# Kernel tuning notes

Hardware: AMD Instinct MI355X
Metric: run time of the kernel (lower is better)

## Reference

```python
import jax, jax.numpy as jnp
import numpy as np

N = 8192      # batch (subjects)
XD = 32       # covariate dim
LD = 32       # encoder latent dim
HD = 128      # odefunc hidden dim
TD = 3        # trans_dim (illness-death model)
NH = 3        # number_of_hazards (allowed transitions)
NP = TD * TD  # num_probs
G = 256       # time grid intervals -> 257 unique times incl. 0
DT = 0.01
STATE = 2 * NP + NH  # [P | P^-1 | cum hazards] = 21


def setup_inputs() -> dict:
    rng = np.random.default_rng(0)
    x = rng.standard_normal((N, XD)).astype(np.float32)
    times = (np.arange(G + 1) * DT).astype(np.float32)  # unique grid incl. t=0
    si = rng.integers(0, G, size=N)
    ei = si + 1 + (rng.random(N) * (G - si)).astype(np.int64)  # ei in (si, G]
    tstart = times[si]
    tstop = times[ei]
    fs = rng.integers(1, 3, size=N)  # from_state in {1,2}
    ts = np.where(fs == 1, rng.integers(2, 4, size=N), 3)  # valid transitions
    # allowed transitions of [[0,1,1],[0,0,1],[0,0,0]]
    trans_rows = np.array([0, 0, 1], dtype=np.int32)
    trans_cols = np.array([1, 2, 2], dtype=np.int32)

    def lin(k, fi, fo, s=1.0):
        r = np.random.default_rng(k)
        return (r.standard_normal((fi, fo)).astype(np.float32) * s / np.sqrt(fi),
                np.zeros(fo, dtype=np.float32))
    enc_W1, enc_b1 = lin(1, XD, 64)
    enc_W2, enc_b2 = lin(2, 64, LD)
    net_W1, net_b1 = lin(3, STATE + LD + XD + 1, HD)
    net_W2, net_b2 = lin(4, HD, 2 * NH, s=0.5)
    return {
        "x": jnp.asarray(x), "tstart": jnp.asarray(tstart), "tstop": jnp.asarray(tstop),
        "from_state": jnp.asarray(fs, jnp.int64), "to_state": jnp.asarray(ts, jnp.int64),
        "tstart_idx": jnp.asarray(si, jnp.int64), "tstop_idx": jnp.asarray(ei, jnp.int64),
        "times": jnp.asarray(times), "trans_rows": jnp.asarray(trans_rows),
        "trans_cols": jnp.asarray(trans_cols),
        "enc_W1": jnp.asarray(enc_W1), "enc_b1": jnp.asarray(enc_b1),
        "enc_W2": jnp.asarray(enc_W2), "enc_b2": jnp.asarray(enc_b2),
        "net_W1": jnp.asarray(net_W1), "net_b1": jnp.asarray(net_b1),
        "net_W2": jnp.asarray(net_W2), "net_b2": jnp.asarray(net_b2),
    }


def reference(x, tstart, tstop, from_state, to_state, tstart_idx, tstop_idx, times,
              trans_rows, trans_cols, enc_W1, enc_b1, enc_W2, enc_b2,
              net_W1, net_b1, net_W2, net_b2):
    n = x.shape[0]
    z = jnp.tanh(x @ enc_W1 + enc_b1) @ enc_W2 + enc_b2  # encoder(x): [n, LD]

    def net(h):  # odefunc.net
        return jnp.tanh(h @ net_W1 + net_b1) @ net_W2 + net_b2

    di = jnp.arange(TD)

    def qmat(qvec, with_diag):
        # scatter hazards into [n,3,3] transition-rate matrix (mask positions)
        Q = jnp.zeros((n, TD, TD), qvec.dtype).at[:, trans_rows, trans_cols].set(qvec)
        if with_diag:
            Q = Q.at[:, di, di].set(-jnp.sum(Q, axis=-1))
        return Q

    # ODE state: [ vec(P(0,t)) | vec(P(0,t)^-1) | cumulative hazards ]
    P0 = jnp.tile(jnp.eye(TD, dtype=x.dtype).reshape(-1), (n, 1))
    state0 = jnp.concatenate([P0, P0, jnp.zeros((n, NH), x.dtype)], axis=1)

    def deriv(state, t):
        P = state[:, :NP].reshape(n, TD, TD)
        Tinv = state[:, NP:2 * NP].reshape(n, TD, TD)
        h = jnp.concatenate([state, z, x, jnp.full((n, 1), t, x.dtype)], axis=1)
        qvec = jax.nn.softplus(net(h)[:, :NH])  # softplus_beta = 1
        Q = qmat(qvec, True)
        dP = jnp.einsum('nij,njk->nik', P, Q)      # dP/dt = P Q
        dTinv = -jnp.einsum('nij,njk->nik', Q, Tinv)  # d(P^-1)/dt = -Q P^-1
        return jnp.concatenate([dP.reshape(n, -1), dTinv.reshape(n, -1), qvec], axis=1)

    def step(state, tdt):
        t, dt = tdt
        new = state + dt * deriv(state, t)  # explicit Euler on the event grid
        return new, new

    dts = times[1:] - times[:-1]
    _, outs = jax.lax.scan(step, state0, (times[:-1], dts))
    out = jnp.concatenate([state0[None], outs], axis=0)  # [T, n, STATE]

    ar = jnp.arange(n)
    # vectorized replacement of the per-sample python-loop gathers
    Tinv_start = out[tstart_idx, ar, NP:2 * NP].reshape(n, TD, TD)
    T_stop = out[tstop_idx, ar, :NP].reshape(n, TD, TD)
    Sfull = jnp.einsum('nij,njk->nik', Tinv_start, T_stop)
    fi = from_state - 1
    ti = to_state - 1
    S = Sfull[ar, fi, fi]

    state_stop = out[tstop_idx, ar, :]
    h1 = jnp.concatenate([state_stop, z, x, tstop[:, None]], axis=1)
    qvec = jax.nn.softplus(net(h1)[:, :NH])
    q = qmat(qvec, False)  # forward() does NOT fill the diagonal here
    lam = q[ar, fi, ti]

    h2 = jnp.concatenate([out[-1], z, x, jnp.full((n, 1), jnp.max(tstop), x.dtype)], axis=1)
    all_hazards_T = net(h2)[:, NH:]
    return S, lam, all_hazards_T
```

## Files before the change

kernel.cpp:

```cpp
#include <hip/hip_runtime.h>

#define NSAMP 8192
#define GSTEP 256
#define SCL   2.8853900817779268f
#define L2E   1.4426950408889634f
#define LN2   0.69314718055994531f
#define LN2DT 0.0069314718055994531f

typedef __attribute__((ext_vector_type(8))) short short8;
typedef __attribute__((ext_vector_type(4))) float f32x4;

__device__ __forceinline__ float exp2_hw(float x){ float r; asm("v_exp_f32 %0, %1" : "=v"(r) : "v"(x)); return r; }
__device__ __forceinline__ float log2_hw(float x){ float r; asm("v_log_f32 %0, %1" : "=v"(r) : "v"(x)); return r; }
__device__ __forceinline__ unsigned pk_bf16(float a, float b){ unsigned r; asm("v_cvt_pk_bf16_f32 %0, %1, %2" : "=v"(r) : "v"(a), "v"(b)); return r; }

__device__ __forceinline__ float tanh_scl(float y) {
    float e = exp2_hw(y);
    return fmaf(-2.0f, __builtin_amdgcn_rcpf(1.0f + e), 1.0f);
}
__device__ __forceinline__ float fast_tanh(float x) {
    float e = exp2_hw(x * SCL);
    return fmaf(-2.0f, __builtin_amdgcn_rcpf(1.0f + e), 1.0f);
}

union frag_u { unsigned u[4]; short8 s; };

__device__ __forceinline__ void split8(const float* v, short8& H, short8& L) {
    frag_u Hu, Lu;
    #pragma unroll
    for (int r = 0; r < 4; ++r) {
        float a = v[2*r], b = v[2*r+1];
        unsigned h = pk_bf16(a, b);
        float ha = __int_as_float(h << 16);
        float hb = __int_as_float(h & 0xffff0000u);
        Hu.u[r] = h;
        Lu.u[r] = pk_bf16(a - ha, b - hb);
    }
    H = Hu.s; L = Lu.s;
}

__global__ void tmax_k(const float* __restrict__ tstop, float* __restrict__ ws) {
    __shared__ float sm[16];
    float m = -1e30f;
    for (int i = threadIdx.x; i < NSAMP; i += 1024) m = fmaxf(m, tstop[i]);
    #pragma unroll
    for (int o = 32; o > 0; o >>= 1) m = fmaxf(m, __shfl_down(m, o, 64));
    if ((threadIdx.x & 63) == 0) sm[threadIdx.x >> 6] = m;
    __syncthreads();
    if (threadIdx.x == 0) {
        float r = sm[0];
        for (int w = 1; w < 16; ++w) r = fmaxf(r, sm[w]);
        ws[0] = r;
    }
}

__global__ void enc_k(const float* __restrict__ x,
                      const float* __restrict__ eW1, const float* __restrict__ eb1,
                      const float* __restrict__ eW2, const float* __restrict__ eb2,
                      float* __restrict__ zout) {
    int s = blockIdx.x * 256 + threadIdx.x;
    float xv[32];
    #pragma unroll
    for (int i = 0; i < 8; ++i) {
        float4 v = reinterpret_cast<const float4*>(x)[s * 8 + i];
        xv[4*i+0] = v.x; xv[4*i+1] = v.y; xv[4*i+2] = v.z; xv[4*i+3] = v.w;
    }
    float z[32];
    #pragma unroll
    for (int o = 0; o < 32; ++o) z[o] = eb2[o];
    #pragma unroll 4
    for (int h = 0; h < 64; ++h) {
        float a = eb1[h];
        #pragma unroll
        for (int i = 0; i < 32; ++i) a += xv[i] * eW1[i * 64 + h];
        float th = fast_tanh(a);
        #pragma unroll
        for (int o = 0; o < 32; ++o) z[o] += th * eW2[h * 32 + o];
    }
    #pragma unroll
    for (int o = 0; o < 32; ++o) zout[s * 32 + o] = z[o];
}

__global__ void __launch_bounds__(64, 1)
surv_k(const float* __restrict__ x,
       const float* __restrict__ tstop,
       const int* __restrict__ fsv, const int* __restrict__ tsv,
       const int* __restrict__ siv, const int* __restrict__ eiv,
       const float* __restrict__ W1, const float* __restrict__ b1,
       const float* __restrict__ W2, const float* __restrict__ b2,
       const float* __restrict__ wsf,
       float* __restrict__ out)
{
    const int l   = threadIdx.x;
    const int a   = l >> 4;
    const int col = l & 15;
    const int s   = blockIdx.x * 16 + col;

    short8 A1h[8], A1l[8];
    #pragma unroll
    for (int tt = 0; tt < 8; ++tt) {
        float av[8];
        #pragma unroll
        for (int i = 0; i < 8; ++i) {
            int k = a * 8 + i;
            float v = 0.f;
            if (k < 21) v = W1[k * 128 + tt * 16 + col];
            else if (k == 21) v = W1[85 * 128 + tt * 16 + col];
            av[i] = v * SCL;
        }
        split8(av, A1h[tt], A1l[tt]);
    }

    short8 A2f[4];
    {
        int  cc  = (col < 6) ? col : 0;
        bool cok = (col < 6);
        float csc = (col < 3) ? L2E : 1.0f;
        #pragma unroll
        for (int j = 0; j < 4; ++j) {
            frag_u F;
            #pragma unroll
            for (int rr = 0; rr < 4; ++rr) {
                int e0 = 2 * rr, e1 = e0 + 1;
                int h0 = j * 32 + (e0 >> 2) * 16 + a * 4 + (e0 & 3);
                int h1 = j * 32 + (e1 >> 2) * 16 + a * 4 + (e1 & 3);
                float w0 = cok ? W2[h0 * 6 + cc] * csc : 0.f;
                float w1 = cok ? W2[h1 * 6 + cc] * csc : 0.f;
                F.u[rr] = pk_bf16(w0, w1);
            }
            A2f[j] = F.s;
        }
    }
    float c2i[4];
    #pragma unroll
    for (int r = 0; r < 4; ++r) {
        int row = a * 4 + r;
        float bv = (row < 6) ? b2[row] : 0.f;
        c2i[r] = (row < 3) ? bv * L2E : bv;
    }

    f32x4 cf[8];
    #pragma unroll
    for (int tt = 0; tt < 8; ++tt) {
        cf[tt] = f32x4{ b1[tt*16 + a*4 + 0], b1[tt*16 + a*4 + 1],
                        b1[tt*16 + a*4 + 2], b1[tt*16 + a*4 + 3] };
    }
    {
        const float* zp = wsf + 16 + s * 32;
        const float* xp = x + s * 32;
        #pragma unroll
        for (int j = 0; j < 2; ++j) {
            float bv[8];
            #pragma unroll
            for (int i = 0; i < 8; ++i) bv[i] = (j == 0) ? zp[a*8 + i] : xp[a*8 + i];
            short8 Bh, Bl; split8(bv, Bh, Bl);
            #pragma unroll
            for (int tt = 0; tt < 8; ++tt) {
                float av[8];
                #pragma unroll
                for (int i = 0; i < 8; ++i)
                    av[i] = W1[(21 + j*32 + a*8 + i) * 128 + tt * 16 + col];
                short8 Ah, Al; split8(av, Ah, Al);
                cf[tt] = __builtin_amdgcn_mfma_f32_16x16x32_bf16(Ah, Bh, cf[tt], 0,0,0);
                cf[tt] = __builtin_amdgcn_mfma_f32_16x16x32_bf16(Ah, Bl, cf[tt], 0,0,0);
                cf[tt] = __builtin_amdgcn_mfma_f32_16x16x32_bf16(Al, Bh, cf[tt], 0,0,0);
            }
        }
        #pragma unroll
        for (int tt = 0; tt < 8; ++tt)
            #pragma unroll
            for (int r = 0; r < 4; ++r) cf[tt][r] *= SCL;
    }

    auto run_net = [&](const float* hs) -> f32x4 {
        float sv[8];
        #pragma unroll
        for (int i = 0; i < 8; ++i) {
            float x01 = (a == 0) ? hs[i] : hs[8 + i];
            float x2  = (i < 6) ? hs[16 + i] : 0.f;
            sv[i] = (a < 2) ? x01 : ((a == 2) ? x2 : 0.f);
        }
        short8 Bh, Bl; split8(sv, Bh, Bl);
        f32x4 acc[8];
        #pragma unroll
        for (int tt = 0; tt < 8; ++tt) {
            acc[tt] = cf[tt];
            acc[tt] = __builtin_amdgcn_mfma_f32_16x16x32_bf16(A1h[tt], Bh, acc[tt], 0,0,0);
            acc[tt] = __builtin_amdgcn_mfma_f32_16x16x32_bf16(A1h[tt], Bl, acc[tt], 0,0,0);
            acc[tt] = __builtin_amdgcn_mfma_f32_16x16x32_bf16(A1l[tt], Bh, acc[tt], 0,0,0);
        }
        f32x4 a2 = { c2i[0], c2i[1], c2i[2], c2i[3] };
        #pragma unroll
        for (int j = 0; j < 4; ++j) {
            frag_u F;
            #pragma unroll
            for (int rr = 0; rr < 4; ++rr) {
                int tile = 2 * j + (rr >> 1);
                int r0 = 2 * (rr & 1);
                F.u[rr] = pk_bf16(tanh_scl(acc[tile][r0]), tanh_scl(acc[tile][r0 + 1]));
            }
            a2 = __builtin_amdgcn_mfma_f32_16x16x32_bf16(A2f[j], F.s, a2, 0,0,0);
        }
        return a2;
    };

    const int si = siv[s], ei = eiv[s];

    float st[22];
    #pragma unroll
    for (int k = 0; k < 22; ++k) st[k] = 0.f;
    st[0] = st[4] = st[8] = 1.f;
    st[9] = st[13] = st[17] = 1.f;
    float Tsnap[9], Ssnap[21];
    #pragma unroll
    for (int k = 0; k < 9; ++k) Tsnap[k] = 0.f;
    #pragma unroll
    for (int k = 0; k < 21; ++k) Ssnap[k] = 0.f;

    for (int m = 0; m < GSTEP; ++m) {
        if (__any((m == si) || (m == ei))) {
            if (m == si) {
                #pragma unroll
                for (int k = 0; k < 9; ++k) Tsnap[k] = st[9 + k];
            }
            if (m == ei) {
                #pragma unroll
                for (int k = 0; k < 21; ++k) Ssnap[k] = st[k];
            }
        }
        st[21] = (float)m * 0.01f;

        f32x4 a2 = run_net(st);
        float y0 = __shfl(a2[0], col, 64);
        float y1 = __shfl(a2[1], col, 64);
        float y2 = __shfl(a2[2], col, 64);
        float q0d = LN2DT * log2_hw(1.0f + exp2_hw(y0));
        float q1d = LN2DT * log2_hw(1.0f + exp2_hw(y1));
        float q2d = LN2DT * log2_hw(1.0f + exp2_hw(y2));
        float qsd = q0d + q1d;

        #pragma unroll
        for (int i = 0; i < 3; ++i) {
            float Pi0 = st[3*i], Pi1 = st[3*i+1];
            st[3*i+0] = fmaf(-qsd, Pi0, st[3*i+0]);
            st[3*i+1] = fmaf(-q2d, Pi1, fmaf(q0d, Pi0, st[3*i+1]));
            st[3*i+2] = fmaf( q2d, Pi1, fmaf(q1d, Pi0, st[3*i+2]));
        }
        #pragma unroll
        for (int k = 0; k < 3; ++k) {
            float T0 = st[9+k], T1 = st[12+k], T2 = st[15+k];
            st[9+k]  = fmaf(-q1d, T2, fmaf(-q0d, T1, fmaf(qsd, T0, st[9+k])));
            st[12+k] = fmaf(q2d, T1 - T2, st[12+k]);
        }
        st[18] += q0d; st[19] += q1d; st[20] += q2d;
    }
    if (ei == GSTEP) {
        #pragma unroll
        for (int k = 0; k < 21; ++k) Ssnap[k] = st[k];
    }

    float h1[22];
    #pragma unroll
    for (int k = 0; k < 21; ++k) h1[k] = Ssnap[k];
    h1[21] = tstop[s];
    f32x4 e1 = run_net(h1);
    float ya = __shfl(e1[0], col, 64);
    float yb = __shfl(e1[1], col, 64);
    float yc = __shfl(e1[2], col, 64);
    float qv0 = LN2 * log2_hw(1.0f + exp2_hw(ya));
    float qv1 = LN2 * log2_hw(1.0f + exp2_hw(yb));
    float qv2 = LN2 * log2_hw(1.0f + exp2_hw(yc));

    float h2[22];
    #pragma unroll
    for (int k = 0; k < 21; ++k) h2[k] = st[k];
    h2[21] = wsf[0];
    f32x4 e2 = run_net(h2);
    float hz3 = __shfl(e2[3], col, 64);
    float hz4 = __shfl(e2[0], 16 + col, 64);
    float hz5 = __shfl(e2[1], 16 + col, 64);

    int fi = fsv[s] - 1;
    int ti = tsv[s] - 1;
    float Sv = 0.f;
    #pragma unroll
    for (int j = 0; j < 3; ++j)
        Sv = fmaf(Tsnap[fi * 3 + j], Ssnap[3 * j + fi], Sv);
    float lam = (fi == 0) ? ((ti == 1) ? qv0 : ((ti == 2) ? qv1 : 0.0f))
                          : ((fi == 1 && ti == 2) ? qv2 : 0.0f);

    if (l < 16) {
        out[s]                     = Sv;
        out[NSAMP + s]             = lam;
        out[2 * NSAMP + 3 * s + 0] = hz3;
        out[2 * NSAMP + 3 * s + 1] = hz4;
        out[2 * NSAMP + 3 * s + 2] = hz5;
    }
}

extern "C" void kernel_launch(void* const* d_in, const int* in_sizes, int n_in,
                              void* d_out, int out_size, void* d_ws, size_t ws_size,
                              hipStream_t stream) {
    const float* x     = (const float*)d_in[0];
    const float* tstop = (const float*)d_in[2];
    const int*   fs    = (const int*)d_in[3];
    const int*   ts    = (const int*)d_in[4];
    const int*   si    = (const int*)d_in[5];
    const int*   ei    = (const int*)d_in[6];
    const float* eW1   = (const float*)d_in[10];
    const float* eb1   = (const float*)d_in[11];
    const float* eW2   = (const float*)d_in[12];
    const float* eb2   = (const float*)d_in[13];
    const float* W1    = (const float*)d_in[14];
    const float* b1    = (const float*)d_in[15];
    const float* W2    = (const float*)d_in[16];
    const float* b2    = (const float*)d_in[17];
    float* wsf = (float*)d_ws;
    float* out = (float*)d_out;

    tmax_k<<<1, 1024, 0, stream>>>(tstop, wsf);
    enc_k<<<32, 256, 0, stream>>>(x, eW1, eb1, eW2, eb2, wsf + 16);
    surv_k<<<512, 64, 0, stream>>>(x, tstop, fs, ts, si, ei,
                                   W1, b1, W2, b2, wsf, out);
}
```

Before: 381.1 us.

## Split hidden layer across two wavefronts per block with LDS reduction

Each block now runs two wavefronts, and each one computes half of the 128 hidden units (4 MFMA tiles instead of 8) for the same 16 samples. Their partial second-layer outputs are combined through a double-buffered shared-memory exchange with a barrier on every Euler step. This halves the serial MFMA and tanh chain per step and doubles the wavefronts on the GPU, since only 512 single-wave blocks ran before. The cost is a __syncthreads plus LDS traffic on each of the 256 steps, and the Euler state update is computed redundantly in both waves.

```diff
diff --git a/kernel.cpp b/kernel.cpp
--- a/kernel.cpp
+++ b/kernel.cpp
@@ -81,7 +81,7 @@
     for (int o = 0; o < 32; ++o) zout[s * 32 + o] = z[o];
 }
 
-__global__ void __launch_bounds__(64, 1)
+__global__ void __launch_bounds__(128, 1)
 surv_k(const float* __restrict__ x,
        const float* __restrict__ tstop,
        const int* __restrict__ fsv, const int* __restrict__ tsv,
@@ -91,39 +91,43 @@
        const float* __restrict__ wsf,
        float* __restrict__ out)
 {
-    const int l   = threadIdx.x;
+    __shared__ __align__(16) float qx[2][2][16][4];
+    const int tid = threadIdx.x;
+    const int wv  = tid >> 6;
+    const int l   = tid & 63;
     const int a   = l >> 4;
     const int col = l & 15;
     const int s   = blockIdx.x * 16 + col;
 
-    short8 A1h[8], A1l[8];
-    #pragma unroll
-    for (int tt = 0; tt < 8; ++tt) {
+    short8 A1h[4], A1l[4];
+    #pragma unroll
+    for (int tt = 0; tt < 4; ++tt) {
+        const int tg = 4 * wv + tt;
         float av[8];
         #pragma unroll
         for (int i = 0; i < 8; ++i) {
             int k = a * 8 + i;
             float v = 0.f;
-            if (k < 21) v = W1[k * 128 + tt * 16 + col];
-            else if (k == 21) v = W1[85 * 128 + tt * 16 + col];
+            if (k < 21) v = W1[k * 128 + tg * 16 + col];
+            else if (k == 21) v = W1[85 * 128 + tg * 16 + col];
             av[i] = v * SCL;
         }
         split8(av, A1h[tt], A1l[tt]);
     }
 
-    short8 A2f[4];
+    short8 A2f[2];
     {
         int  cc  = (col < 6) ? col : 0;
         bool cok = (col < 6);
         float csc = (col < 3) ? L2E : 1.0f;
         #pragma unroll
-        for (int j = 0; j < 4; ++j) {
+        for (int j = 0; j < 2; ++j) {
             frag_u F;
             #pragma unroll
             for (int rr = 0; rr < 4; ++rr) {
                 int e0 = 2 * rr, e1 = e0 + 1;
-                int h0 = j * 32 + (e0 >> 2) * 16 + a * 4 + (e0 & 3);
-                int h1 = j * 32 + (e1 >> 2) * 16 + a * 4 + (e1 & 3);
+                int h0 = (2 * wv + j) * 32 + (e0 >> 2) * 16 + a * 4 + (e0 & 3);
+                int h1 = (2 * wv + j) * 32 + (e1 >> 2) * 16 + a * 4 + (e1 & 3);
                 float w0 = cok ? W2[h0 * 6 + cc] * csc : 0.f;
                 float w1 = cok ? W2[h1 * 6 + cc] * csc : 0.f;
                 F.u[rr] = pk_bf16(w0, w1);
@@ -131,19 +135,14 @@
             A2f[j] = F.s;
         }
     }
-    float c2i[4];
-    #pragma unroll
-    for (int r = 0; r < 4; ++r) {
-        int row = a * 4 + r;
-        float bv = (row < 6) ? b2[row] : 0.f;
-        c2i[r] = (row < 3) ? bv * L2E : bv;
-    }
-
-    f32x4 cf[8];
-    #pragma unroll
-    for (int tt = 0; tt < 8; ++tt) {
-        cf[tt] = f32x4{ b1[tt*16 + a*4 + 0], b1[tt*16 + a*4 + 1],
-                        b1[tt*16 + a*4 + 2], b1[tt*16 + a*4 + 3] };
+    const float sb0 = L2E * b2[0], sb1 = L2E * b2[1], sb2 = L2E * b2[2];
+
+    f32x4 cf[4];
+    #pragma unroll
+    for (int tt = 0; tt < 4; ++tt) {
+        const int tg = 4 * wv + tt;
+        cf[tt] = f32x4{ b1[tg*16 + a*4 + 0], b1[tg*16 + a*4 + 1],
+                        b1[tg*16 + a*4 + 2], b1[tg*16 + a*4 + 3] };
     }
     {
         const float* zp = wsf + 16 + s * 32;
@@ -155,11 +154,12 @@
             for (int i = 0; i < 8; ++i) bv[i] = (j == 0) ? zp[a*8 + i] : xp[a*8 + i];
             short8 Bh, Bl; split8(bv, Bh, Bl);
             #pragma unroll
-            for (int tt = 0; tt < 8; ++tt) {
+            for (int tt = 0; tt < 4; ++tt) {
+                const int tg = 4 * wv + tt;
                 float av[8];
                 #pragma unroll
                 for (int i = 0; i < 8; ++i)
-                    av[i] = W1[(21 + j*32 + a*8 + i) * 128 + tt * 16 + col];
+                    av[i] = W1[(21 + j*32 + a*8 + i) * 128 + tg * 16 + col];
                 short8 Ah, Al; split8(av, Ah, Al);
                 cf[tt] = __builtin_amdgcn_mfma_f32_16x16x32_bf16(Ah, Bh, cf[tt], 0,0,0);
                 cf[tt] = __builtin_amdgcn_mfma_f32_16x16x32_bf16(Ah, Bl, cf[tt], 0,0,0);
@@ -167,7 +167,7 @@
             }
         }
         #pragma unroll
-        for (int tt = 0; tt < 8; ++tt)
+        for (int tt = 0; tt < 4; ++tt)
             #pragma unroll
             for (int r = 0; r < 4; ++r) cf[tt][r] *= SCL;
     }
@@ -181,17 +181,17 @@
             sv[i] = (a < 2) ? x01 : ((a == 2) ? x2 : 0.f);
         }
         short8 Bh, Bl; split8(sv, Bh, Bl);
-        f32x4 acc[8];
-        #pragma unroll
-        for (int tt = 0; tt < 8; ++tt) {
+        f32x4 acc[4];
+        #pragma unroll
+        for (int tt = 0; tt < 4; ++tt) {
             acc[tt] = cf[tt];
             acc[tt] = __builtin_amdgcn_mfma_f32_16x16x32_bf16(A1h[tt], Bh, acc[tt], 0,0,0);
             acc[tt] = __builtin_amdgcn_mfma_f32_16x16x32_bf16(A1h[tt], Bl, acc[tt], 0,0,0);
             acc[tt] = __builtin_amdgcn_mfma_f32_16x16x32_bf16(A1l[tt], Bh, acc[tt], 0,0,0);
         }
-        f32x4 a2 = { c2i[0], c2i[1], c2i[2], c2i[3] };
-        #pragma unroll
-        for (int j = 0; j < 4; ++j) {
+        f32x4 a2 = {0.f, 0.f, 0.f, 0.f};
+        #pragma unroll
+        for (int j = 0; j < 2; ++j) {
             frag_u F;
             #pragma unroll
             for (int rr = 0; rr < 4; ++rr) {
@@ -217,6 +217,7 @@
     #pragma unroll
     for (int k = 0; k < 21; ++k) Ssnap[k] = 0.f;
 
+    int buf = 0;
     for (int m = 0; m < GSTEP; ++m) {
         if (__any((m == si) || (m == ei))) {
             if (m == si) {
@@ -231,12 +232,16 @@
         st[21] = (float)m * 0.01f;
 
         f32x4 a2 = run_net(st);
-        float y0 = __shfl(a2[0], col, 64);
-        float y1 = __shfl(a2[1], col, 64);
-        float y2 = __shfl(a2[2], col, 64);
-        float q0d = LN2DT * log2_hw(1.0f + exp2_hw(y0));
-        float q1d = LN2DT * log2_hw(1.0f + exp2_hw(y1));
-        float q2d = LN2DT * log2_hw(1.0f + exp2_hw(y2));
+        if (l < 16)
+            *reinterpret_cast<float4*>(&qx[buf][wv][col][0]) =
+                make_float4(a2[0], a2[1], a2[2], 0.f);
+        __syncthreads();
+        float4 pA = *reinterpret_cast<const float4*>(&qx[buf][0][col][0]);
+        float4 pB = *reinterpret_cast<const float4*>(&qx[buf][1][col][0]);
+        buf ^= 1;
+        float q0d = LN2DT * log2_hw(1.0f + exp2_hw(pA.x + pB.x + sb0));
+        float q1d = LN2DT * log2_hw(1.0f + exp2_hw(pA.y + pB.y + sb1));
+        float q2d = LN2DT * log2_hw(1.0f + exp2_hw(pA.z + pB.z + sb2));
         float qsd = q0d + q1d;
 
         #pragma unroll
@@ -259,26 +264,35 @@
         for (int k = 0; k < 21; ++k) Ssnap[k] = st[k];
     }
 
+    __syncthreads();
+
     float h1[22];
     #pragma unroll
     for (int k = 0; k < 21; ++k) h1[k] = Ssnap[k];
     h1[21] = tstop[s];
     f32x4 e1 = run_net(h1);
-    float ya = __shfl(e1[0], col, 64);
-    float yb = __shfl(e1[1], col, 64);
-    float yc = __shfl(e1[2], col, 64);
+    if (l < 16)
+        *reinterpret_cast<float4*>(&qx[0][wv][col][0]) =
+            make_float4(e1[0], e1[1], e1[2], 0.f);
+
+    float h2[22];
+    #pragma unroll
+    for (int k = 0; k < 21; ++k) h2[k] = st[k];
+    h2[21] = wsf[0];
+    f32x4 e2 = run_net(h2);
+    if (a == 0) qx[1][wv][col][0] = e2[3];
+    if (a == 1) { qx[1][wv][col][1] = e2[0]; qx[1][wv][col][2] = e2[1]; }
+    __syncthreads();
+
+    float ya = qx[0][0][col][0] + qx[0][1][col][0] + sb0;
+    float yb = qx[0][0][col][1] + qx[0][1][col][1] + sb1;
+    float yc = qx[0][0][col][2] + qx[0][1][col][2] + sb2;
     float qv0 = LN2 * log2_hw(1.0f + exp2_hw(ya));
     float qv1 = LN2 * log2_hw(1.0f + exp2_hw(yb));
     float qv2 = LN2 * log2_hw(1.0f + exp2_hw(yc));
-
-    float h2[22];
-    #pragma unroll
-    for (int k = 0; k < 21; ++k) h2[k] = st[k];
-    h2[21] = wsf[0];
-    f32x4 e2 = run_net(h2);
-    float hz3 = __shfl(e2[3], col, 64);
-    float hz4 = __shfl(e2[0], 16 + col, 64);
-    float hz5 = __shfl(e2[1], 16 + col, 64);
+    float hz3 = qx[1][0][col][0] + qx[1][1][col][0] + b2[3];
+    float hz4 = qx[1][0][col][1] + qx[1][1][col][1] + b2[4];
+    float hz5 = qx[1][0][col][2] + qx[1][1][col][2] + b2[5];
 
     int fi = fsv[s] - 1;
     int ti = tsv[s] - 1;
@@ -289,7 +303,7 @@
     float lam = (fi == 0) ? ((ti == 1) ? qv0 : ((ti == 2) ? qv1 : 0.0f))
                           : ((fi == 1 && ti == 2) ? qv2 : 0.0f);
 
-    if (l < 16) {
+    if (wv == 0 && l < 16) {
         out[s]                     = Sv;
         out[NSAMP + s]             = lam;
         out[2 * NSAMP + 3 * s + 0] = hz3;
@@ -320,6 +334,6 @@
 
     tmax_k<<<1, 1024, 0, stream>>>(tstop, wsf);
     enc_k<<<32, 256, 0, stream>>>(x, eW1, eb1, eW2, eb2, wsf + 16);
-    surv_k<<<512, 64, 0, stream>>>(x, tstop, fs, ts, si, ei,
-                                   W1, b1, W2, b2, wsf, out);
-}
+    surv_k<<<512, 128, 0, stream>>>(x, tstop, fs, ts, si, ei,
+                                    W1, b1, W2, b2, wsf, out);
+}
```

Result: slower. 427.4 us (+12.2%).

## Replace layer-2 MFMA with fp32 FMA dot using tanh = 1 - 2u identity

Applied to the files above, without the earlier changes.

Rewrites the second layer so it no longer runs bf16 MFMAs over padded 16-wide tiles. Each lane computes u = 1/(1+exp2(y)) and accumulates three fp32 FMAs against weights pre-scaled by -2*log2(e). The constant part of tanh (the column sums of W2) is folded into the bias, and cross-lane shuffles reduce the partial sums. This removes the bf16 packing, the tanh finishing FMA and the MFMA dependency chain per step, and it also raises layer-2 precision to fp32. The cost is 96 extra weight registers per lane and a shuffle reduction on every step.

```diff
diff --git a/kernel.cpp b/kernel.cpp
--- a/kernel.cpp
+++ b/kernel.cpp
@@ -14,9 +14,8 @@
 __device__ __forceinline__ float log2_hw(float x){ float r; asm("v_log_f32 %0, %1" : "=v"(r) : "v"(x)); return r; }
 __device__ __forceinline__ unsigned pk_bf16(float a, float b){ unsigned r; asm("v_cvt_pk_bf16_f32 %0, %1, %2" : "=v"(r) : "v"(a), "v"(b)); return r; }
 
-__device__ __forceinline__ float tanh_scl(float y) {
-    float e = exp2_hw(y);
-    return fmaf(-2.0f, __builtin_amdgcn_rcpf(1.0f + e), 1.0f);
+__device__ __forceinline__ float u_of(float y) {
+    return __builtin_amdgcn_rcpf(1.0f + exp2_hw(y));
 }
 __device__ __forceinline__ float fast_tanh(float x) {
     float e = exp2_hw(x * SCL);
@@ -111,33 +110,32 @@
         split8(av, A1h[tt], A1l[tt]);
     }
 
-    short8 A2f[4];
-    {
-        int  cc  = (col < 6) ? col : 0;
-        bool cok = (col < 6);
-        float csc = (col < 3) ? L2E : 1.0f;
-        #pragma unroll
-        for (int j = 0; j < 4; ++j) {
-            frag_u F;
-            #pragma unroll
-            for (int rr = 0; rr < 4; ++rr) {
-                int e0 = 2 * rr, e1 = e0 + 1;
-                int h0 = j * 32 + (e0 >> 2) * 16 + a * 4 + (e0 & 3);
-                int h1 = j * 32 + (e1 >> 2) * 16 + a * 4 + (e1 & 3);
-                float w0 = cok ? W2[h0 * 6 + cc] * csc : 0.f;
-                float w1 = cok ? W2[h1 * 6 + cc] * csc : 0.f;
-                F.u[rr] = pk_bf16(w0, w1);
-            }
-            A2f[j] = F.s;
-        }
-    }
-    float c2i[4];
-    #pragma unroll
-    for (int r = 0; r < 4; ++r) {
-        int row = a * 4 + r;
-        float bv = (row < 6) ? b2[row] : 0.f;
-        c2i[r] = (row < 3) ? bv * L2E : bv;
-    }
+    float W2n[8][4][3];
+    float rs0 = 0.f, rs1 = 0.f, rs2 = 0.f, rs3 = 0.f, rs4 = 0.f, rs5 = 0.f;
+    #pragma unroll
+    for (int tt = 0; tt < 8; ++tt)
+        #pragma unroll
+        for (int r = 0; r < 4; ++r) {
+            int jd = tt * 16 + a * 4 + r;
+            float w0 = W2[jd * 6 + 0], w1 = W2[jd * 6 + 1], w2 = W2[jd * 6 + 2];
+            rs0 += w0; rs1 += w1; rs2 += w2;
+            rs3 += W2[jd * 6 + 3]; rs4 += W2[jd * 6 + 4]; rs5 += W2[jd * 6 + 5];
+            W2n[tt][r][0] = -2.f * L2E * w0;
+            W2n[tt][r][1] = -2.f * L2E * w1;
+            W2n[tt][r][2] = -2.f * L2E * w2;
+        }
+    rs0 += __shfl_xor(rs0, 16, 64); rs0 += __shfl_xor(rs0, 32, 64);
+    rs1 += __shfl_xor(rs1, 16, 64); rs1 += __shfl_xor(rs1, 32, 64);
+    rs2 += __shfl_xor(rs2, 16, 64); rs2 += __shfl_xor(rs2, 32, 64);
+    rs3 += __shfl_xor(rs3, 16, 64); rs3 += __shfl_xor(rs3, 32, 64);
+    rs4 += __shfl_xor(rs4, 16, 64); rs4 += __shfl_xor(rs4, 32, 64);
+    rs5 += __shfl_xor(rs5, 16, 64); rs5 += __shfl_xor(rs5, 32, 64);
+    const float SB0 = L2E * (b2[0] + rs0);
+    const float SB1 = L2E * (b2[1] + rs1);
+    const float SB2 = L2E * (b2[2] + rs2);
+    const float SBe3 = b2[3] + rs3;
+    const float SBe4 = b2[4] + rs4;
+    const float SBe5 = b2[5] + rs5;
 
     f32x4 cf[8];
     #pragma unroll
@@ -172,7 +170,7 @@
             for (int r = 0; r < 4; ++r) cf[tt][r] *= SCL;
     }
 
-    auto run_net = [&](const float* hs) -> f32x4 {
+    auto run_l1 = [&](const float* hs, f32x4* acc) {
         float sv[8];
         #pragma unroll
         for (int i = 0; i < 8; ++i) {
@@ -181,7 +179,6 @@
             sv[i] = (a < 2) ? x01 : ((a == 2) ? x2 : 0.f);
         }
         short8 Bh, Bl; split8(sv, Bh, Bl);
-        f32x4 acc[8];
         #pragma unroll
         for (int tt = 0; tt < 8; ++tt) {
             acc[tt] = cf[tt];
@@ -189,19 +186,6 @@
             acc[tt] = __builtin_amdgcn_mfma_f32_16x16x32_bf16(A1h[tt], Bl, acc[tt], 0,0,0);
             acc[tt] = __builtin_amdgcn_mfma_f32_16x16x32_bf16(A1l[tt], Bh, acc[tt], 0,0,0);
         }
-        f32x4 a2 = { c2i[0], c2i[1], c2i[2], c2i[3] };
-        #pragma unroll
-        for (int j = 0; j < 4; ++j) {
-            frag_u F;
-            #pragma unroll
-            for (int rr = 0; rr < 4; ++rr) {
-                int tile = 2 * j + (rr >> 1);
-                int r0 = 2 * (rr & 1);
-                F.u[rr] = pk_bf16(tanh_scl(acc[tile][r0]), tanh_scl(acc[tile][r0 + 1]));
-            }
-            a2 = __builtin_amdgcn_mfma_f32_16x16x32_bf16(A2f[j], F.s, a2, 0,0,0);
-        }
-        return a2;
     };
 
     const int si = siv[s], ei = eiv[s];
@@ -230,13 +214,24 @@
         }
         st[21] = (float)m * 0.01f;
 
-        f32x4 a2 = run_net(st);
-        float y0 = __shfl(a2[0], col, 64);
-        float y1 = __shfl(a2[1], col, 64);
-        float y2 = __shfl(a2[2], col, 64);
-        float q0d = LN2DT * log2_hw(1.0f + exp2_hw(y0));
-        float q1d = LN2DT * log2_hw(1.0f + exp2_hw(y1));
-        float q2d = LN2DT * log2_hw(1.0f + exp2_hw(y2));
+        f32x4 acc[8];
+        run_l1(st, acc);
+        float p0 = 0.f, p1 = 0.f, p2 = 0.f;
+        #pragma unroll
+        for (int tt = 0; tt < 8; ++tt)
+            #pragma unroll
+            for (int r = 0; r < 4; ++r) {
+                float u = u_of(acc[tt][r]);
+                p0 = fmaf(u, W2n[tt][r][0], p0);
+                p1 = fmaf(u, W2n[tt][r][1], p1);
+                p2 = fmaf(u, W2n[tt][r][2], p2);
+            }
+        p0 += __shfl_xor(p0, 16, 64); p0 += __shfl_xor(p0, 32, 64);
+        p1 += __shfl_xor(p1, 16, 64); p1 += __shfl_xor(p1, 32, 64);
+        p2 += __shfl_xor(p2, 16, 64); p2 += __shfl_xor(p2, 32, 64);
+        float q0d = LN2DT * log2_hw(1.0f + exp2_hw(p0 + SB0));
+        float q1d = LN2DT * log2_hw(1.0f + exp2_hw(p1 + SB1));
+        float q2d = LN2DT * log2_hw(1.0f + exp2_hw(p2 + SB2));
         float qsd = q0d + q1d;
 
         #pragma unroll
@@ -263,22 +258,54 @@
     #pragma unroll
     for (int k = 0; k < 21; ++k) h1[k] = Ssnap[k];
     h1[21] = tstop[s];
-    f32x4 e1 = run_net(h1);
-    float ya = __shfl(e1[0], col, 64);
-    float yb = __shfl(e1[1], col, 64);
-    float yc = __shfl(e1[2], col, 64);
-    float qv0 = LN2 * log2_hw(1.0f + exp2_hw(ya));
-    float qv1 = LN2 * log2_hw(1.0f + exp2_hw(yb));
-    float qv2 = LN2 * log2_hw(1.0f + exp2_hw(yc));
+    float qv0, qv1, qv2;
+    {
+        f32x4 acc[8];
+        run_l1(h1, acc);
+        float p0 = 0.f, p1 = 0.f, p2 = 0.f;
+        #pragma unroll
+        for (int tt = 0; tt < 8; ++tt)
+            #pragma unroll
+            for (int r = 0; r < 4; ++r) {
+                float u = u_of(acc[tt][r]);
+                p0 = fmaf(u, W2n[tt][r][0], p0);
+                p1 = fmaf(u, W2n[tt][r][1], p1);
+                p2 = fmaf(u, W2n[tt][r][2], p2);
+            }
+        p0 += __shfl_xor(p0, 16, 64); p0 += __shfl_xor(p0, 32, 64);
+        p1 += __shfl_xor(p1, 16, 64); p1 += __shfl_xor(p1, 32, 64);
+        p2 += __shfl_xor(p2, 16, 64); p2 += __shfl_xor(p2, 32, 64);
+        qv0 = LN2 * log2_hw(1.0f + exp2_hw(p0 + SB0));
+        qv1 = LN2 * log2_hw(1.0f + exp2_hw(p1 + SB1));
+        qv2 = LN2 * log2_hw(1.0f + exp2_hw(p2 + SB2));
+    }
 
     float h2[22];
     #pragma unroll
     for (int k = 0; k < 21; ++k) h2[k] = st[k];
     h2[21] = wsf[0];
-    f32x4 e2 = run_net(h2);
-    float hz3 = __shfl(e2[3], col, 64);
-    float hz4 = __shfl(e2[0], 16 + col, 64);
-    float hz5 = __shfl(e2[1], 16 + col, 64);
+    float hz3, hz4, hz5;
+    {
+        f32x4 acc[8];
+        run_l1(h2, acc);
+        float p3 = 0.f, p4 = 0.f, p5 = 0.f;
+        #pragma unroll
+        for (int tt = 0; tt < 8; ++tt)
+            #pragma unroll
+            for (int r = 0; r < 4; ++r) {
+                int jd = tt * 16 + a * 4 + r;
+                float u = u_of(acc[tt][r]);
+                p3 = fmaf(u, -2.f * W2[jd * 6 + 3], p3);
+                p4 = fmaf(u, -2.f * W2[jd * 6 + 4], p4);
+                p5 = fmaf(u, -2.f * W2[jd * 6 + 5], p5);
+            }
+        p3 += __shfl_xor(p3, 16, 64); p3 += __shfl_xor(p3, 32, 64);
+        p4 += __shfl_xor(p4, 16, 64); p4 += __shfl_xor(p4, 32, 64);
+        p5 += __shfl_xor(p5, 16, 64); p5 += __shfl_xor(p5, 32, 64);
+        hz3 = p3 + SBe3;
+        hz4 = p4 + SBe4;
+        hz5 = p5 + SBe5;
+    }
 
     int fi = fsv[s] - 1;
     int ti = tsv[s] - 1;
```

Result: no change. 380.4 us (-0.2%).
